# Kernel optimization log

Hardware: AMD Instinct MI355X
Metric: run time of the kernel (lower is better)

## Reference

```python
import jax, jax.numpy as jnp
import numpy as np

N = 4096        # number of cells (graph nodes)
D = 128         # feature / embedding dim (isize)
NEIGHBOR = 15   # kNN column used for the distance cutoff
GAMMA = 8.0
OMEGA = 0.5


def setup_inputs() -> dict:
    key = jax.random.key(0)
    k = jax.random.split(key, 6)
    features = jax.random.normal(k[0], (N, D), dtype=jnp.float32)
    # sparse binary adjacency (~16 neighbors/node on average), stored dense
    adj = (jax.random.uniform(k[1], (N, N)) < 0.004).astype(jnp.float32)
    # symmetric positive pairwise distances
    d = jax.random.uniform(k[2], (N, N), minval=0.05, maxval=1.0)
    dis = ((d + d.T) * 0.5).astype(jnp.float32)
    scale = 1.0 / np.sqrt(D)
    W0 = (jax.random.normal(k[3], (D, D), dtype=jnp.float32) * scale)
    b0 = jnp.zeros((D,), jnp.float32)
    W1 = (jax.random.normal(k[4], (D, D), dtype=jnp.float32) * scale)
    b1 = jnp.zeros((D,), jnp.float32)
    return {"features": features, "adj": adj, "dis": dis,
            "W0": W0, "b0": b0, "W1": W1, "b1": b1}


def _gcn_layer(h, A, W, b):
    # torch_geometric GCNConv: sym-normalize (A + I), then X' = A_norm @ X @ W + b
    A_hat = A + jnp.eye(A.shape[0], dtype=A.dtype)
    deg = A_hat.sum(axis=1)
    dinv = jnp.where(deg > 0, 1.0 / jnp.sqrt(deg), 0.0)
    A_norm = dinv[:, None] * A_hat * dinv[None, :]
    return A_norm @ (h @ W) + b


def reference(features, adj, dis, W0, b0, W1, b1):
    eps = 1e-8
    # --- buffers precomputed in __init__ of the torch module ---
    d_sorted = jnp.sort(dis, axis=1)
    d_cut = jnp.median(d_sorted[:, NEIGHBOR])
    adj_mask = (dis > 0) & (dis <= d_cut)
    d_scaled = jnp.where(adj_mask, dis, jnp.inf) / d_cut
    s_d = jnp.exp(-GAMMA * d_scaled * d_scaled)   # 1/exp(g*d^2); exp(-inf)=0
    # --- internal_forward: 2 GCN layers on adj.T, relu between ---
    A = adj.T
    h = jax.nn.relu(_gcn_layer(features, A, W0, b0))
    h = _gcn_layer(h, A, W1, b1)
    # --- masked cosine similarity, blend with distance kernel ---
    h_norm = jnp.linalg.norm(h, axis=1, keepdims=True)   # [N,1]
    s1 = (h @ h.T) / (h_norm @ h_norm.T + eps)
    s1 = jnp.maximum(s1, 0.0)
    s = OMEGA * s1 + (1.0 - OMEGA) * s_d
    s = jnp.where(adj_mask, s, 0.0)
    # --- symmetric degree normalization D^{-1/2} S D^{-1/2} ---
    deg = s.sum(axis=1)
    dinv = jnp.where(deg > 0, 1.0 / jnp.sqrt(deg), 0.0)
    s_norm = dinv[:, None] * s * dinv[None, :]
    return s_norm, s
```

## Files before the change

kernel.cpp:

```cpp
#include <hip/hip_runtime.h>

#define N 4096
#define CAP 128

__global__ __launch_bounds__(256) void k_build(const float4* __restrict__ adj4,
                                               int* __restrict__ cnt1,
                                               int* __restrict__ nbr1) {
  int idx = blockIdx.x * blockDim.x + threadIdx.x;
  int stride = gridDim.x * blockDim.x;
  int total = N * N / 4;
  for (int k = idx; k < total; k += stride) {
    float4 a = adj4[k];
    int base = k << 2;
    int j  = base >> 12;
    int i0 = base & (N - 1);
    if (a.x != 0.f) { int p = atomicAdd(&cnt1[i0 + 0], 1); if (p < CAP) nbr1[(i0 + 0) * CAP + p] = j; }
    if (a.y != 0.f) { int p = atomicAdd(&cnt1[i0 + 1], 1); if (p < CAP) nbr1[(i0 + 1) * CAP + p] = j; }
    if (a.z != 0.f) { int p = atomicAdd(&cnt1[i0 + 2], 1); if (p < CAP) nbr1[(i0 + 2) * CAP + p] = j; }
    if (a.w != 0.f) { int p = atomicAdd(&cnt1[i0 + 3], 1); if (p < CAP) nbr1[(i0 + 3) * CAP + p] = j; }
  }
}

__global__ __launch_bounds__(256) void k_dinv1(const int* __restrict__ cnt1, float* __restrict__ dinv1) {
  int i = blockIdx.x * 256 + threadIdx.x;
  if (i < N) dinv1[i] = 1.0f / sqrtf((float)cnt1[i] + 1.0f);
}

__global__ __launch_bounds__(256) void k_row16(const float* __restrict__ dis, float* __restrict__ r16) {
  int row = blockIdx.x;
  int t = threadIdx.x;
  const float* rp = dis + (size_t)row * N;
  float v[16];
#pragma unroll
  for (int q = 0; q < 16; q++) v[q] = rp[q * 256 + t];

#pragma unroll
  for (int k = 2; k <= 16; k <<= 1) {
#pragma unroll
    for (int d = k >> 1; d > 0; d >>= 1) {
#pragma unroll
      for (int i = 0; i < 16; i++) {
        int l = i ^ d;
        if (l > i) {
          bool up = ((i & k) == 0);
          float a = v[i], b = v[l];
          bool sw = up ? (a > b) : (a < b);
          float lo = sw ? b : a, hi = sw ? a : b;
          v[i] = lo; v[l] = hi;
        }
      }
    }
  }

#pragma unroll
  for (int s = 1; s <= 32; s <<= 1) {
    float r[16];
#pragma unroll
    for (int i = 0; i < 16; i++) r[i] = __shfl_xor(v[i], s, 64);
    float w[16];
#pragma unroll
    for (int i = 0; i < 16; i++) w[i] = fminf(v[i], r[15 - i]);
#pragma unroll
    for (int d = 8; d > 0; d >>= 1) {
#pragma unroll
      for (int i = 0; i < 16; i++) {
        int l = i ^ d;
        if (l > i) {
          float a = w[i], b = w[l];
          w[i] = fminf(a, b); w[l] = fmaxf(a, b);
        }
      }
    }
#pragma unroll
    for (int i = 0; i < 16; i++) v[i] = w[i];
  }

  __shared__ float sw4[4][16];
  int wv = t >> 6;
  if ((t & 63) == 0) {
#pragma unroll
    for (int i = 0; i < 16; i++) sw4[wv][i] = v[i];
  }
  __syncthreads();
  if (t == 0) {
    int p0 = 0, p1 = 0, p2 = 0, p3 = 0;
    float m = 0.f;
    for (int c = 0; c < 16; c++) {
      float h0 = sw4[0][p0], h1 = sw4[1][p1], h2 = sw4[2][p2], h3 = sw4[3][p3];
      m = fminf(fminf(h0, h1), fminf(h2, h3));
      if      (m == h0) p0++;
      else if (m == h1) p1++;
      else if (m == h2) p2++;
      else              p3++;
    }
    r16[row] = m;
  }
}

__global__ __launch_bounds__(1024) void k_median(const float* __restrict__ r16, float* __restrict__ scal) {
  __shared__ float sh[N];
  int t = threadIdx.x;
  for (int i = t; i < N; i += 1024) sh[i] = r16[i];
  __syncthreads();
  for (int k = 2; k <= N; k <<= 1) {
    for (int d = k >> 1; d > 0; d >>= 1) {
      for (int i = t; i < N; i += 1024) {
        int l = i ^ d;
        if (l > i) {
          bool up = ((i & k) == 0);
          float x = sh[i], y = sh[l];
          if (up ? (x > y) : (x < y)) { sh[i] = y; sh[l] = x; }
        }
      }
      __syncthreads();
    }
  }
  if (t == 0) {
    float dcut = 0.5f * (sh[2047] + sh[2048]);
    scal[0] = dcut;
    scal[1] = 1.0f / dcut;
  }
}

__global__ __launch_bounds__(128) void k_gemm128(const float* __restrict__ X, const float* __restrict__ W,
                                                 const float* __restrict__ dinv, float* __restrict__ out) {
  __shared__ float xs[8][128];
  int t = threadIdx.x;
  int r0 = blockIdx.x * 8;
#pragma unroll
  for (int r = 0; r < 8; r++) xs[r][t] = X[(size_t)(r0 + r) * 128 + t];
  __syncthreads();
  float acc[8] = {0.f, 0.f, 0.f, 0.f, 0.f, 0.f, 0.f, 0.f};
#pragma unroll 4
  for (int k = 0; k < 128; k++) {
    float wk = W[k * 128 + t];
#pragma unroll
    for (int r = 0; r < 8; r++) acc[r] = fmaf(xs[r][k], wk, acc[r]);
  }
#pragma unroll
  for (int r = 0; r < 8; r++) out[(size_t)(r0 + r) * 128 + t] = dinv[r0 + r] * acc[r];
}

__global__ __launch_bounds__(128) void k_spmm_relu(const float* __restrict__ Yd, const int* __restrict__ cnt,
                                                   const int* __restrict__ nbr, const float* __restrict__ dinv,
                                                   const float* __restrict__ b, float* __restrict__ hout) {
  int row = blockIdx.x, t = threadIdx.x;
  int c = min(cnt[row], CAP);
  const int* lst = nbr + row * CAP;
  float acc = Yd[(size_t)row * 128 + t];
  for (int q = 0; q < c; q++) {
    int j = lst[q];
    acc += Yd[(size_t)j * 128 + t];
  }
  hout[(size_t)row * 128 + t] = fmaxf(dinv[row] * acc + b[t], 0.0f);
}

__global__ __launch_bounds__(128) void k_spmm_norm(const float* __restrict__ Yd, const int* __restrict__ cnt,
                                                   const int* __restrict__ nbr, const float* __restrict__ dinv,
                                                   const float* __restrict__ b, float* __restrict__ hout,
                                                   float* __restrict__ hnorm) {
  __shared__ float red[2];
  int row = blockIdx.x, t = threadIdx.x;
  int c = min(cnt[row], CAP);
  const int* lst = nbr + row * CAP;
  float acc = Yd[(size_t)row * 128 + t];
  for (int q = 0; q < c; q++) {
    int j = lst[q];
    acc += Yd[(size_t)j * 128 + t];
  }
  float h = dinv[row] * acc + b[t];
  hout[(size_t)row * 128 + t] = h;
  float ss = h * h;
#pragma unroll
  for (int s = 32; s; s >>= 1) ss += __shfl_xor(ss, s, 64);
  if ((t & 63) == 0) red[t >> 6] = ss;
  __syncthreads();
  if (t == 0) hnorm[row] = sqrtf(red[0] + red[1]);
}

__global__ __launch_bounds__(256) void k_phaseA(const float* __restrict__ dis, const float* __restrict__ scal,
                                                float* __restrict__ s_out, int* __restrict__ cnt2,
                                                int* __restrict__ nbr2, float* __restrict__ sdsum) {
  __shared__ int lcnt;
  __shared__ int lidx[CAP];
  __shared__ float lred[4];
  int row = blockIdx.x, t = threadIdx.x;
  if (t == 0) lcnt = 0;
  __syncthreads();
  float dcut = scal[0];
  const float4* dp = (const float4*)(dis + (size_t)row * N);
  float4* sp = (float4*)(s_out + (size_t)row * N);
  float lsum = 0.f;
#pragma unroll
  for (int q = 0; q < 4; q++) {
    int k4 = q * 256 + t;
    float4 d = dp[k4];
    int jb = k4 << 2;
    float4 sv;
    float dd, s;
    dd = d.x; s = 0.f;
    if (dd > 0.f && dd <= dcut) { float r = dd / dcut; s = 0.5f * expf(-8.0f * r * r);
      int p = atomicAdd(&lcnt, 1); if (p < CAP) lidx[p] = jb + 0; lsum += s; }
    sv.x = s;
    dd = d.y; s = 0.f;
    if (dd > 0.f && dd <= dcut) { float r = dd / dcut; s = 0.5f * expf(-8.0f * r * r);
      int p = atomicAdd(&lcnt, 1); if (p < CAP) lidx[p] = jb + 1; lsum += s; }
    sv.y = s;
    dd = d.z; s = 0.f;
    if (dd > 0.f && dd <= dcut) { float r = dd / dcut; s = 0.5f * expf(-8.0f * r * r);
      int p = atomicAdd(&lcnt, 1); if (p < CAP) lidx[p] = jb + 2; lsum += s; }
    sv.z = s;
    dd = d.w; s = 0.f;
    if (dd > 0.f && dd <= dcut) { float r = dd / dcut; s = 0.5f * expf(-8.0f * r * r);
      int p = atomicAdd(&lcnt, 1); if (p < CAP) lidx[p] = jb + 3; lsum += s; }
    sv.w = s;
    sp[k4] = sv;
  }
#pragma unroll
  for (int s = 32; s; s >>= 1) lsum += __shfl_xor(lsum, s, 64);
  if ((t & 63) == 0) lred[t >> 6] = lsum;
  __syncthreads();
  int c = lcnt;
  if (t == 0) {
    sdsum[row] = lred[0] + lred[1] + lred[2] + lred[3];
    cnt2[row] = min(c, CAP);
  }
  for (int i = t; i < min(c, CAP); i += 256) nbr2[row * CAP + i] = lidx[i];
}

__global__ __launch_bounds__(256) void k_phaseB(const float* __restrict__ h, const float* __restrict__ hnorm,
                                                const int* __restrict__ cnt2, const int* __restrict__ nbr2,
                                                const float* __restrict__ sdsum, float* __restrict__ s_out,
                                                float* __restrict__ deg) {
  __shared__ float hi[128];
  __shared__ float wred[4];
  int row = blockIdx.x, t = threadIdx.x, wv = t >> 6, ln = t & 63;
  if (t < 128) hi[t] = h[(size_t)row * 128 + t];
  __syncthreads();
  int c = cnt2[row];
  float ni = hnorm[row];
  float wsum = 0.f;
  for (int idx = wv; idx < c; idx += 4) {
    int j = nbr2[row * CAP + idx];
    const float* hj = h + (size_t)j * 128;
    float p = hi[ln] * hj[ln] + hi[ln + 64] * hj[ln + 64];
#pragma unroll
    for (int s = 32; s; s >>= 1) p += __shfl_xor(p, s, 64);
    if (ln == 0) {
      float s1 = fmaxf(p / (ni * hnorm[j] + 1e-8f), 0.f);
      float v = 0.5f * s1;
      s_out[(size_t)row * N + j] += v;
      wsum += v;
    }
  }
  if (ln == 0) wred[wv] = wsum;
  __syncthreads();
  if (t == 0) deg[row] = sdsum[row] + wred[0] + wred[1] + wred[2] + wred[3];
}

__global__ __launch_bounds__(256) void k_dinv2(const float* __restrict__ deg, float* __restrict__ dinv2) {
  int i = blockIdx.x * 256 + threadIdx.x;
  if (i < N) {
    float d = deg[i];
    dinv2[i] = (d > 0.f) ? (1.0f / sqrtf(d)) : 0.f;
  }
}

__global__ __launch_bounds__(256) void k_norm(const float4* __restrict__ s4, const float* __restrict__ dinv2,
                                              float4* __restrict__ o4) {
  int idx = blockIdx.x * 256 + threadIdx.x;
  int i = idx >> 10;
  int jb = idx & 1023;
  float di = dinv2[i];
  float4 dj = ((const float4*)dinv2)[jb];
  float4 v = s4[idx];
  float4 r;
  r.x = di * dj.x * v.x;
  r.y = di * dj.y * v.y;
  r.z = di * dj.z * v.z;
  r.w = di * dj.w * v.w;
  o4[idx] = r;
}

extern "C" void kernel_launch(void* const* d_in, const int* in_sizes, int n_in,
                              void* d_out, int out_size, void* d_ws, size_t ws_size,
                              hipStream_t stream) {
  const float* features = (const float*)d_in[0];
  const float* adj      = (const float*)d_in[1];
  const float* dis      = (const float*)d_in[2];
  const float* W0       = (const float*)d_in[3];
  const float* b0       = (const float*)d_in[4];
  const float* W1       = (const float*)d_in[5];
  const float* b1       = (const float*)d_in[6];
  float* out    = (float*)d_out;
  float* s_half = out + (size_t)N * N;

  char* ws = (char*)d_ws;
  float* r16   = (float*)(ws + 0);
  int*   cnt1  = (int*)  (ws + 16384);
  float* dinv1 = (float*)(ws + 32768);
  float* sdsum = (float*)(ws + 49152);
  float* deg   = (float*)(ws + 65536);
  float* dinv2 = (float*)(ws + 81920);
  int*   cnt2  = (int*)  (ws + 98304);
  float* scal  = (float*)(ws + 114688);
  int*   nbr1  = (int*)  (ws + 131072);
  int*   nbr2  = (int*)  (ws + 131072 + 1 * 2097152);
  float* Yd0   = (float*)(ws + 131072 + 2 * 2097152);
  float* h1    = (float*)(ws + 131072 + 3 * 2097152);
  float* Y1d   = (float*)(ws + 131072 + 4 * 2097152);
  float* hbuf  = (float*)(ws + 131072 + 5 * 2097152);
  float* hnorm = (float*)(ws + 131072 + 6 * 2097152);

  hipMemsetAsync(cnt1, 0, N * sizeof(int), stream);

  k_build<<<2048, 256, 0, stream>>>((const float4*)adj, cnt1, nbr1);
  k_dinv1<<<N / 256, 256, 0, stream>>>(cnt1, dinv1);
  k_row16<<<N, 256, 0, stream>>>(dis, r16);
  k_median<<<1, 1024, 0, stream>>>(r16, scal);
  k_gemm128<<<N / 8, 128, 0, stream>>>(features, W0, dinv1, Yd0);
  k_spmm_relu<<<N, 128, 0, stream>>>(Yd0, cnt1, nbr1, dinv1, b0, h1);
  k_gemm128<<<N / 8, 128, 0, stream>>>(h1, W1, dinv1, Y1d);
  k_spmm_norm<<<N, 128, 0, stream>>>(Y1d, cnt1, nbr1, dinv1, b1, hbuf, hnorm);
  k_phaseA<<<N, 256, 0, stream>>>(dis, scal, s_half, cnt2, nbr2, sdsum);
  k_phaseB<<<N, 256, 0, stream>>>(hbuf, hnorm, cnt2, nbr2, sdsum, s_half, deg);
  k_dinv2<<<N / 256, 256, 0, stream>>>(deg, dinv2);
  k_norm<<<(N * (N / 4)) / 256, 256, 0, stream>>>((const float4*)s_half, dinv2, (float4*)out);
}
```

Measured before the change: 404.7 us.

## Replace bitonic sorts with threshold selection and radix-select median, fuse dinv kernels

The per-row 16th-smallest search swaps a full register bitonic sort for an adaptive threshold filter: it gathers candidates below a threshold into shared memory, then ranks them by counting. The median over 4096 values becomes an 8-bit radix select instead of a 4096-element bitonic sort in one block. The small dinv1 and dinv2 kernels are removed and their values recomputed inline in consumers, saving two launches. The threshold loop may take several passes over the row if the distances are distributed unevenly. k_norm now recomputes rsqrt for every element.

```diff
diff --git a/kernel.cpp b/kernel.cpp
--- a/kernel.cpp
+++ b/kernel.cpp
@@ -21,109 +21,87 @@
   }
 }
 
-__global__ __launch_bounds__(256) void k_dinv1(const int* __restrict__ cnt1, float* __restrict__ dinv1) {
-  int i = blockIdx.x * 256 + threadIdx.x;
-  if (i < N) dinv1[i] = 1.0f / sqrtf((float)cnt1[i] + 1.0f);
-}
-
 __global__ __launch_bounds__(256) void k_row16(const float* __restrict__ dis, float* __restrict__ r16) {
-  int row = blockIdx.x;
+  __shared__ int lcnt;
+  __shared__ float lval[CAP];
+  int row = blockIdx.x, t = threadIdx.x;
+  const float4* dp = (const float4*)(dis + (size_t)row * N);
+  float T = 0.12f;
+  int c = 0;
+  for (int iter = 0; iter < 24; iter++) {
+    if (t == 0) lcnt = 0;
+    __syncthreads();
+#pragma unroll
+    for (int q = 0; q < 4; q++) {
+      float4 d = dp[q * 256 + t];
+      if (d.x <= T) { int p = atomicAdd(&lcnt, 1); if (p < CAP) lval[p] = d.x; }
+      if (d.y <= T) { int p = atomicAdd(&lcnt, 1); if (p < CAP) lval[p] = d.y; }
+      if (d.z <= T) { int p = atomicAdd(&lcnt, 1); if (p < CAP) lval[p] = d.z; }
+      if (d.w <= T) { int p = atomicAdd(&lcnt, 1); if (p < CAP) lval[p] = d.w; }
+    }
+    __syncthreads();
+    c = lcnt;
+    __syncthreads();
+    if (c >= 16 && c <= CAP) break;
+    T = (c < 16) ? T * 2.0f : T * 0.5f;
+  }
+  if (t < c) {
+    float v = lval[t];
+    int less = 0;
+    for (int j = 0; j < c; j++) {
+      float u = lval[j];
+      less += (u < v) || (u == v && j < t);
+    }
+    if (less == 15) r16[row] = v;
+  }
+}
+
+__global__ __launch_bounds__(256) void k_median(const float* __restrict__ r16, float* __restrict__ scal) {
+  __shared__ unsigned int keys[N];
+  __shared__ int hist[256];
+  __shared__ unsigned int s_prefix;
+  __shared__ int s_rank;
   int t = threadIdx.x;
-  const float* rp = dis + (size_t)row * N;
-  float v[16];
-#pragma unroll
-  for (int q = 0; q < 16; q++) v[q] = rp[q * 256 + t];
-
-#pragma unroll
-  for (int k = 2; k <= 16; k <<= 1) {
-#pragma unroll
-    for (int d = k >> 1; d > 0; d >>= 1) {
-#pragma unroll
-      for (int i = 0; i < 16; i++) {
-        int l = i ^ d;
-        if (l > i) {
-          bool up = ((i & k) == 0);
-          float a = v[i], b = v[l];
-          bool sw = up ? (a > b) : (a < b);
-          float lo = sw ? b : a, hi = sw ? a : b;
-          v[i] = lo; v[l] = hi;
-        }
-      }
-    }
-  }
-
-#pragma unroll
-  for (int s = 1; s <= 32; s <<= 1) {
-    float r[16];
-#pragma unroll
-    for (int i = 0; i < 16; i++) r[i] = __shfl_xor(v[i], s, 64);
-    float w[16];
-#pragma unroll
-    for (int i = 0; i < 16; i++) w[i] = fminf(v[i], r[15 - i]);
-#pragma unroll
-    for (int d = 8; d > 0; d >>= 1) {
-#pragma unroll
-      for (int i = 0; i < 16; i++) {
-        int l = i ^ d;
-        if (l > i) {
-          float a = w[i], b = w[l];
-          w[i] = fminf(a, b); w[l] = fmaxf(a, b);
-        }
-      }
-    }
-#pragma unroll
-    for (int i = 0; i < 16; i++) v[i] = w[i];
-  }
-
-  __shared__ float sw4[4][16];
-  int wv = t >> 6;
-  if ((t & 63) == 0) {
-#pragma unroll
-    for (int i = 0; i < 16; i++) sw4[wv][i] = v[i];
-  }
-  __syncthreads();
-  if (t == 0) {
-    int p0 = 0, p1 = 0, p2 = 0, p3 = 0;
-    float m = 0.f;
-    for (int c = 0; c < 16; c++) {
-      float h0 = sw4[0][p0], h1 = sw4[1][p1], h2 = sw4[2][p2], h3 = sw4[3][p3];
-      m = fminf(fminf(h0, h1), fminf(h2, h3));
-      if      (m == h0) p0++;
-      else if (m == h1) p1++;
-      else if (m == h2) p2++;
-      else              p3++;
-    }
-    r16[row] = m;
-  }
-}
-
-__global__ __launch_bounds__(1024) void k_median(const float* __restrict__ r16, float* __restrict__ scal) {
-  __shared__ float sh[N];
-  int t = threadIdx.x;
-  for (int i = t; i < N; i += 1024) sh[i] = r16[i];
-  __syncthreads();
-  for (int k = 2; k <= N; k <<= 1) {
-    for (int d = k >> 1; d > 0; d >>= 1) {
-      for (int i = t; i < N; i += 1024) {
-        int l = i ^ d;
-        if (l > i) {
-          bool up = ((i & k) == 0);
-          float x = sh[i], y = sh[l];
-          if (up ? (x > y) : (x < y)) { sh[i] = y; sh[l] = x; }
-        }
+#pragma unroll
+  for (int q = 0; q < 16; q++) keys[q * 256 + t] = __float_as_uint(r16[q * 256 + t]);
+  __syncthreads();
+  float res[2];
+#pragma unroll
+  for (int sel = 0; sel < 2; sel++) {
+    if (t == 0) { s_rank = 2047 + sel; s_prefix = 0u; }
+    __syncthreads();
+    unsigned int mask = 0u;
+    for (int shift = 24; shift >= 0; shift -= 8) {
+      hist[t] = 0;
+      __syncthreads();
+      unsigned int prefix = s_prefix;
+#pragma unroll
+      for (int q = 0; q < 16; q++) {
+        unsigned int k = keys[q * 256 + t];
+        if ((k & mask) == prefix) atomicAdd(&hist[(k >> shift) & 255], 1);
       }
       __syncthreads();
+      if (t == 0) {
+        int r = s_rank, acc = 0, b = 0;
+        for (; b < 256; b++) { if (acc + hist[b] > r) break; acc += hist[b]; }
+        s_prefix = prefix | ((unsigned int)b << shift);
+        s_rank = r - acc;
+      }
+      __syncthreads();
+      mask |= (255u << shift);
     }
+    res[sel] = __uint_as_float(s_prefix);
+    __syncthreads();
   }
   if (t == 0) {
-    float dcut = 0.5f * (sh[2047] + sh[2048]);
+    float dcut = 0.5f * (res[0] + res[1]);
     scal[0] = dcut;
     scal[1] = 1.0f / dcut;
   }
 }
 
 __global__ __launch_bounds__(128) void k_gemm128(const float* __restrict__ X, const float* __restrict__ W,
-                                                 const float* __restrict__ dinv, float* __restrict__ out) {
+                                                 const int* __restrict__ cnt1, float* __restrict__ out) {
   __shared__ float xs[8][128];
   int t = threadIdx.x;
   int r0 = blockIdx.x * 8;
@@ -138,11 +116,14 @@
     for (int r = 0; r < 8; r++) acc[r] = fmaf(xs[r][k], wk, acc[r]);
   }
 #pragma unroll
-  for (int r = 0; r < 8; r++) out[(size_t)(r0 + r) * 128 + t] = dinv[r0 + r] * acc[r];
+  for (int r = 0; r < 8; r++) {
+    float dv = 1.0f / sqrtf((float)cnt1[r0 + r] + 1.0f);
+    out[(size_t)(r0 + r) * 128 + t] = dv * acc[r];
+  }
 }
 
 __global__ __launch_bounds__(128) void k_spmm_relu(const float* __restrict__ Yd, const int* __restrict__ cnt,
-                                                   const int* __restrict__ nbr, const float* __restrict__ dinv,
+                                                   const int* __restrict__ nbr,
                                                    const float* __restrict__ b, float* __restrict__ hout) {
   int row = blockIdx.x, t = threadIdx.x;
   int c = min(cnt[row], CAP);
@@ -152,11 +133,12 @@
     int j = lst[q];
     acc += Yd[(size_t)j * 128 + t];
   }
-  hout[(size_t)row * 128 + t] = fmaxf(dinv[row] * acc + b[t], 0.0f);
+  float dv = 1.0f / sqrtf((float)c + 1.0f);
+  hout[(size_t)row * 128 + t] = fmaxf(dv * acc + b[t], 0.0f);
 }
 
 __global__ __launch_bounds__(128) void k_spmm_norm(const float* __restrict__ Yd, const int* __restrict__ cnt,
-                                                   const int* __restrict__ nbr, const float* __restrict__ dinv,
+                                                   const int* __restrict__ nbr,
                                                    const float* __restrict__ b, float* __restrict__ hout,
                                                    float* __restrict__ hnorm) {
   __shared__ float red[2];
@@ -168,7 +150,8 @@
     int j = lst[q];
     acc += Yd[(size_t)j * 128 + t];
   }
-  float h = dinv[row] * acc + b[t];
+  float dv = 1.0f / sqrtf((float)c + 1.0f);
+  float h = dv * acc + b[t];
   hout[(size_t)row * 128 + t] = h;
   float ss = h * h;
 #pragma unroll
@@ -258,27 +241,20 @@
   if (t == 0) deg[row] = sdsum[row] + wred[0] + wred[1] + wred[2] + wred[3];
 }
 
-__global__ __launch_bounds__(256) void k_dinv2(const float* __restrict__ deg, float* __restrict__ dinv2) {
-  int i = blockIdx.x * 256 + threadIdx.x;
-  if (i < N) {
-    float d = deg[i];
-    dinv2[i] = (d > 0.f) ? (1.0f / sqrtf(d)) : 0.f;
-  }
-}
-
-__global__ __launch_bounds__(256) void k_norm(const float4* __restrict__ s4, const float* __restrict__ dinv2,
+__global__ __launch_bounds__(256) void k_norm(const float4* __restrict__ s4, const float* __restrict__ deg,
                                               float4* __restrict__ o4) {
   int idx = blockIdx.x * 256 + threadIdx.x;
   int i = idx >> 10;
   int jb = idx & 1023;
-  float di = dinv2[i];
-  float4 dj = ((const float4*)dinv2)[jb];
+  float dgi = deg[i];
+  float di = (dgi > 0.f) ? (1.0f / sqrtf(dgi)) : 0.f;
+  float4 dg = ((const float4*)deg)[jb];
   float4 v = s4[idx];
   float4 r;
-  r.x = di * dj.x * v.x;
-  r.y = di * dj.y * v.y;
-  r.z = di * dj.z * v.z;
-  r.w = di * dj.w * v.w;
+  r.x = di * ((dg.x > 0.f) ? (1.0f / sqrtf(dg.x)) : 0.f) * v.x;
+  r.y = di * ((dg.y > 0.f) ? (1.0f / sqrtf(dg.y)) : 0.f) * v.y;
+  r.z = di * ((dg.z > 0.f) ? (1.0f / sqrtf(dg.z)) : 0.f) * v.z;
+  r.w = di * ((dg.w > 0.f) ? (1.0f / sqrtf(dg.w)) : 0.f) * v.w;
   o4[idx] = r;
 }
 
@@ -288,8 +264,8 @@
   const float* features = (const float*)d_in[0];
   const float* adj      = (const float*)d_in[1];
   const float* dis      = (const float*)d_in[2];
+  const float* b0       = (const float*)d_in[4];
   const float* W0       = (const float*)d_in[3];
-  const float* b0       = (const float*)d_in[4];
   const float* W1       = (const float*)d_in[5];
   const float* b1       = (const float*)d_in[6];
   float* out    = (float*)d_out;
@@ -298,10 +274,8 @@
   char* ws = (char*)d_ws;
   float* r16   = (float*)(ws + 0);
   int*   cnt1  = (int*)  (ws + 16384);
-  float* dinv1 = (float*)(ws + 32768);
   float* sdsum = (float*)(ws + 49152);
   float* deg   = (float*)(ws + 65536);
-  float* dinv2 = (float*)(ws + 81920);
   int*   cnt2  = (int*)  (ws + 98304);
   float* scal  = (float*)(ws + 114688);
   int*   nbr1  = (int*)  (ws + 131072);
@@ -315,15 +289,13 @@
   hipMemsetAsync(cnt1, 0, N * sizeof(int), stream);
 
   k_build<<<2048, 256, 0, stream>>>((const float4*)adj, cnt1, nbr1);
-  k_dinv1<<<N / 256, 256, 0, stream>>>(cnt1, dinv1);
   k_row16<<<N, 256, 0, stream>>>(dis, r16);
-  k_median<<<1, 1024, 0, stream>>>(r16, scal);
-  k_gemm128<<<N / 8, 128, 0, stream>>>(features, W0, dinv1, Yd0);
-  k_spmm_relu<<<N, 128, 0, stream>>>(Yd0, cnt1, nbr1, dinv1, b0, h1);
-  k_gemm128<<<N / 8, 128, 0, stream>>>(h1, W1, dinv1, Y1d);
-  k_spmm_norm<<<N, 128, 0, stream>>>(Y1d, cnt1, nbr1, dinv1, b1, hbuf, hnorm);
+  k_median<<<1, 256, 0, stream>>>(r16, scal);
+  k_gemm128<<<N / 8, 128, 0, stream>>>(features, W0, cnt1, Yd0);
+  k_spmm_relu<<<N, 128, 0, stream>>>(Yd0, cnt1, nbr1, b0, h1);
+  k_gemm128<<<N / 8, 128, 0, stream>>>(h1, W1, cnt1, Y1d);
+  k_spmm_norm<<<N, 128, 0, stream>>>(Y1d, cnt1, nbr1, b1, hbuf, hnorm);
   k_phaseA<<<N, 256, 0, stream>>>(dis, scal, s_half, cnt2, nbr2, sdsum);
   k_phaseB<<<N, 256, 0, stream>>>(hbuf, hnorm, cnt2, nbr2, sdsum, s_half, deg);
-  k_dinv2<<<N / 256, 256, 0, stream>>>(deg, dinv2);
-  k_norm<<<(N * (N / 4)) / 256, 256, 0, stream>>>((const float4*)s_half, dinv2, (float4*)out);
-}
+  k_norm<<<(N * (N / 4)) / 256, 256, 0, stream>>>((const float4*)s_half, deg, (float4*)out);
+}
```

New measurement: 398.7 us. About the same (-1.5%).
